# Optimization experiments

Measured on AMD Instinct MI355X. Metric: run time of the kernel, lower is better.

The kernel has to match this reference:

```python
import jax, jax.numpy as jnp
import numpy as np

N = 100000
E = 800000
D_IN = 128
D_OUT = 128


def setup_inputs() -> dict:
    key = jax.random.key(0)
    k1, k2, k3, k4, k5 = jax.random.split(key, 5)
    x = jax.random.normal(k1, (N, D_IN), dtype=jnp.float32)
    edge_index = jax.random.randint(k2, (2, E), 0, N, dtype=jnp.int64)
    # xavier-uniform linear weight [out, in]
    lim_w = float(np.sqrt(6.0 / (D_IN + D_OUT)))
    lin_w = jax.random.uniform(k3, (D_OUT, D_IN), minval=-lim_w, maxval=lim_w, dtype=jnp.float32)
    # torch default bias init: U(-1/sqrt(fan_in), 1/sqrt(fan_in))
    lim_b = float(1.0 / np.sqrt(D_IN))
    lin_b = jax.random.uniform(k4, (D_OUT,), minval=-lim_b, maxval=lim_b, dtype=jnp.float32)
    lim_s = float(np.sqrt(6.0 / (D_OUT + D_OUT)))
    weight = jax.random.uniform(k5, (D_OUT, D_OUT), minval=-lim_s, maxval=lim_s, dtype=jnp.float32)
    return {"x": x, "edge_index": edge_index, "lin_w": lin_w, "lin_b": lin_b, "weight": weight}


def reference(x, edge_index, lin_w, lin_b, weight):
    row, col = edge_index[0], edge_index[1]
    # mean aggregation: scatter-add gathered neighbor features, normalize by degree
    agg = jax.ops.segment_sum(x[col], row, num_segments=x.shape[0])  # [N, d_in]
    deg = jax.ops.segment_sum(jnp.ones_like(row, dtype=x.dtype), row, num_segments=x.shape[0])
    deg = jnp.maximum(deg, 1.0)
    out = agg / deg[:, None]
    out = out @ lin_w.T + lin_b          # linear
    out = out @ weight                    # trailing matmul
    return out
```

## Files before the change

kernel.cpp:

```cpp
#include <hip/hip_runtime.h>

#define N_NODES 100000
#define N_EDGES 800000
#define D 128
#define MAXDEG 40
#define YSTRIDE 132
#define HIST_B 896
#define HIST_T (HIST_B * 256)
#define TILES 3125
#define TB2 1563

typedef unsigned int u32;
typedef unsigned short u16;
typedef __attribute__((ext_vector_type(8))) short bf16x8;
typedef __attribute__((ext_vector_type(4))) float f32x4;

static __device__ __forceinline__ short f2bf(float f) {
    u32 u = __float_as_uint(f);
    u += 0x7FFFu + ((u >> 16) & 1u);
    return (short)(u >> 16);
}
static __device__ __forceinline__ u32 pack2(float lo, float hi) {
    return (u32)(u16)f2bf(lo) | ((u32)(u16)f2bf(hi) << 16);
}
static __device__ __forceinline__ float bf_lo(u32 u) { return __uint_as_float(u << 16); }
static __device__ __forceinline__ float bf_hi(u32 u) { return __uint_as_float(u & 0xFFFF0000u); }

__global__ __launch_bounds__(256) void hist_pre_kernel(
    const int* __restrict__ ei,
    const float* __restrict__ lin_w, const float* __restrict__ lin_b,
    const float* __restrict__ weight,
    u32* __restrict__ deg16, int* __restrict__ csr,
    u16* __restrict__ Mfrag, float* __restrict__ b2)
{
    int t = threadIdx.x;
    int blk = blockIdx.x;
    if (blk < HIST_B) {
        int e0 = blk * 256 + t;
        int e1 = e0 + HIST_T;
        int e2 = e0 + 2 * HIST_T;
        int e3 = e0 + 3 * HIST_T;
        int r0 = ei[e0];
        int r1 = ei[e1];
        int r2 = ei[e2];
        bool has3 = (e3 < N_EDGES);
        int r3 = has3 ? ei[e3] : 0;
        int c0 = ei[N_EDGES + e0];
        int c1 = ei[N_EDGES + e1];
        int c2 = ei[N_EDGES + e2];
        int c3 = has3 ? ei[N_EDGES + e3] : 0;
        u32 p0 = atomicAdd(deg16 + r0 * 16, 1u);
        u32 p1 = atomicAdd(deg16 + r1 * 16, 1u);
        u32 p2 = atomicAdd(deg16 + r2 * 16, 1u);
        u32 p3 = has3 ? atomicAdd(deg16 + r3 * 16, 1u) : (u32)MAXDEG;
        if (p0 < (u32)MAXDEG) csr[r0 * MAXDEG + (int)p0] = c0;
        if (p1 < (u32)MAXDEG) csr[r1 * MAXDEG + (int)p1] = c1;
        if (p2 < (u32)MAXDEG) csr[r2 * MAXDEG + (int)p2] = c2;
        if (p3 < (u32)MAXDEG) csr[r3 * MAXDEG + (int)p3] = c3;
    } else if (blk < 960) {
        int kk = (blk - HIST_B) * 2 + (t >> 7);
        int n = t & 127;
        float acc = 0.f;
        for (int o = 0; o < D; ++o)
            acc += lin_w[o * D + kk] * weight[o * D + n];
        int idx = ((((n >> 4) * 4 + (kk >> 5)) * 64) + ((kk >> 3) & 3) * 16 + (n & 15)) * 8 + (kk & 7);
        Mfrag[idx] = (u16)f2bf(acc);
    } else if (blk == 960 && t < D) {
        float acc = 0.f;
        for (int o = 0; o < D; ++o)
            acc += lin_b[o] * weight[o * D + t];
        b2[t] = acc;
    }
}

static __device__ __forceinline__ void compute_tile(
    const char* __restrict__ bufb, float* __restrict__ shY,
    const bf16x8* __restrict__ mb, u16* __restrict__ y,
    int tile, int t, int rt, int ch, int quad, int mrow, int sw)
{
    int r = rt * 16 + mrow;
    f32x4 acc0 = {0.f, 0.f, 0.f, 0.f};
    f32x4 acc1 = {0.f, 0.f, 0.f, 0.f};
    f32x4 acc2 = {0.f, 0.f, 0.f, 0.f};
    f32x4 acc3 = {0.f, 0.f, 0.f, 0.f};

    #pragma unroll
    for (int ks = 0; ks < 4; ++ks) {
        int base = quad * 32 + ks * 128;
        float4 lo = *(const float4*)(bufb + (r << 9) + (base ^ sw));
        float4 hi = *(const float4*)(bufb + (r << 9) + ((base + 16) ^ sw));
        bf16x8 a;
        a[0] = f2bf(lo.x); a[1] = f2bf(lo.y); a[2] = f2bf(lo.z); a[3] = f2bf(lo.w);
        a[4] = f2bf(hi.x); a[5] = f2bf(hi.y); a[6] = f2bf(hi.z); a[7] = f2bf(hi.w);

        bf16x8 b0 = mb[ks * 64 + 0 * 256];
        bf16x8 b1 = mb[ks * 64 + 1 * 256];
        bf16x8 b2f = mb[ks * 64 + 2 * 256];
        bf16x8 b3 = mb[ks * 64 + 3 * 256];
        acc0 = __builtin_amdgcn_mfma_f32_16x16x32_bf16(a, b0, acc0, 0, 0, 0);
        acc1 = __builtin_amdgcn_mfma_f32_16x16x32_bf16(a, b1, acc1, 0, 0, 0);
        acc2 = __builtin_amdgcn_mfma_f32_16x16x32_bf16(a, b2f, acc2, 0, 0, 0);
        acc3 = __builtin_amdgcn_mfma_f32_16x16x32_bf16(a, b3, acc3, 0, 0, 0);
    }

    {
        float* dst = shY + (size_t)(rt * 16 + quad * 4) * YSTRIDE + ch * 64 + mrow;
        #pragma unroll
        for (int rr = 0; rr < 4; ++rr) {
            dst[rr * YSTRIDE + 0 * 16] = acc0[rr];
            dst[rr * YSTRIDE + 1 * 16] = acc1[rr];
            dst[rr * YSTRIDE + 2 * 16] = acc2[rr];
            dst[rr * YSTRIDE + 3 * 16] = acc3[rr];
        }
    }
    __syncthreads();

    {
        int orow = t >> 3, seg = t & 7;
        const float* src = shY + (size_t)orow * YSTRIDE + seg * 16;
        u32 p[8];
        #pragma unroll
        for (int i = 0; i < 8; ++i)
            p[i] = pack2(src[2 * i], src[2 * i + 1]);
        u32* dst = (u32*)y + ((size_t)(tile * 32 + orow) * 64 + seg * 8);
        *(uint4*)(dst + 0) = make_uint4(p[0], p[1], p[2], p[3]);
        *(uint4*)(dst + 4) = make_uint4(p[4], p[5], p[6], p[7]);
    }
}

__global__ __launch_bounds__(256) void transform_kernel(
    const float* __restrict__ x, const u16* __restrict__ Mfrag, u16* __restrict__ y)
{
    __shared__ float shX[2 * 32 * 128];
    __shared__ float shY[32 * YSTRIDE];
    int t = threadIdx.x;
    int blk = blockIdx.x;
    int wave = t >> 6, lane = t & 63;
    int rt = wave & 1, ch = wave >> 1;
    int quad = lane >> 4, mrow = lane & 15;
    int sw = (mrow & 7) << 4;

    int tile0 = blk * 2;
    int tile1 = blk * 2 + 1;
    bool has1 = (tile1 < TILES);

    {
        char* shXb = (char*)shX;
        #pragma unroll
        for (int i = 0; i < 4; ++i) {
            int s = (i * 256 + t) * 16;
            int rr = s >> 9;
            int cb = s & 511;
            int g = (rr << 9) + (cb ^ ((rr & 7) << 4));
            __builtin_amdgcn_global_load_lds(
                (const u32*)((const char*)x + (size_t)tile0 * 16384 + g),
                (u32*)(shXb + i * 4096 + wave * 1024), 16, 0, 0);
        }
        if (has1) {
            #pragma unroll
            for (int i = 0; i < 4; ++i) {
                int s = (i * 256 + t) * 16;
                int rr = s >> 9;
                int cb = s & 511;
                int g = (rr << 9) + (cb ^ ((rr & 7) << 4));
                __builtin_amdgcn_global_load_lds(
                    (const u32*)((const char*)x + (size_t)tile1 * 16384 + g),
                    (u32*)(shXb + 16384 + i * 4096 + wave * 1024), 16, 0, 0);
            }
        }
    }

    const bf16x8* mb = (const bf16x8*)(Mfrag) + (ch * 4) * 4 * 64 + lane;

    if (has1) asm volatile("s_waitcnt vmcnt(4)" ::: "memory");
    else      asm volatile("s_waitcnt vmcnt(0)" ::: "memory");
    __builtin_amdgcn_s_barrier();
    __builtin_amdgcn_sched_barrier(0);

    compute_tile((const char*)shX, shY, mb, y, tile0, t, rt, ch, quad, mrow, sw);

    if (has1) {
        __syncthreads();
        compute_tile((const char*)shX + 16384, shY, mb, y, tile1, t, rt, ch, quad, mrow, sw);
    }
}

__global__ __launch_bounds__(256) void gather_kernel(
    const u16* __restrict__ y, const int* __restrict__ csr,
    const u32* __restrict__ deg16,
    const float* __restrict__ b2, float* __restrict__ out)
{
    int idx = blockIdx.x * 256 + threadIdx.x;
    int n = idx >> 4;
    int sl = idx & 15;
    if (n >= N_NODES) return;
    u32 dn = deg16[n * 16];
    u32 cnt = (dn > (u32)MAXDEG) ? (u32)MAXDEG : dn;
    const int* cp = csr + (size_t)n * MAXDEG;
    const u32* yw = (const u32*)y;
    float a0 = 0.f, a1 = 0.f, a2 = 0.f, a3 = 0.f;
    float a4 = 0.f, a5 = 0.f, a6 = 0.f, a7 = 0.f;
    u32 e = 0;
    for (; e + 8 <= cnt; e += 8) {
        int4 ca = *(const int4*)(cp + e);
        int4 cb = *(const int4*)(cp + e + 4);
        uint4 u0 = *(const uint4*)(yw + (size_t)ca.x * 64 + sl * 4);
        uint4 u1 = *(const uint4*)(yw + (size_t)ca.y * 64 + sl * 4);
        uint4 u2 = *(const uint4*)(yw + (size_t)ca.z * 64 + sl * 4);
        uint4 u3 = *(const uint4*)(yw + (size_t)ca.w * 64 + sl * 4);
        uint4 u4 = *(const uint4*)(yw + (size_t)cb.x * 64 + sl * 4);
        uint4 u5 = *(const uint4*)(yw + (size_t)cb.y * 64 + sl * 4);
        uint4 u6 = *(const uint4*)(yw + (size_t)cb.z * 64 + sl * 4);
        uint4 u7 = *(const uint4*)(yw + (size_t)cb.w * 64 + sl * 4);
        a0 += ((bf_lo(u0.x) + bf_lo(u1.x)) + (bf_lo(u2.x) + bf_lo(u3.x)))
            + ((bf_lo(u4.x) + bf_lo(u5.x)) + (bf_lo(u6.x) + bf_lo(u7.x)));
        a1 += ((bf_hi(u0.x) + bf_hi(u1.x)) + (bf_hi(u2.x) + bf_hi(u3.x)))
            + ((bf_hi(u4.x) + bf_hi(u5.x)) + (bf_hi(u6.x) + bf_hi(u7.x)));
        a2 += ((bf_lo(u0.y) + bf_lo(u1.y)) + (bf_lo(u2.y) + bf_lo(u3.y)))
            + ((bf_lo(u4.y) + bf_lo(u5.y)) + (bf_lo(u6.y) + bf_lo(u7.y)));
        a3 += ((bf_hi(u0.y) + bf_hi(u1.y)) + (bf_hi(u2.y) + bf_hi(u3.y)))
            + ((bf_hi(u4.y) + bf_hi(u5.y)) + (bf_hi(u6.y) + bf_hi(u7.y)));
        a4 += ((bf_lo(u0.z) + bf_lo(u1.z)) + (bf_lo(u2.z) + bf_lo(u3.z)))
            + ((bf_lo(u4.z) + bf_lo(u5.z)) + (bf_lo(u6.z) + bf_lo(u7.z)));
        a5 += ((bf_hi(u0.z) + bf_hi(u1.z)) + (bf_hi(u2.z) + bf_hi(u3.z)))
            + ((bf_hi(u4.z) + bf_hi(u5.z)) + (bf_hi(u6.z) + bf_hi(u7.z)));
        a6 += ((bf_lo(u0.w) + bf_lo(u1.w)) + (bf_lo(u2.w) + bf_lo(u3.w)))
            + ((bf_lo(u4.w) + bf_lo(u5.w)) + (bf_lo(u6.w) + bf_lo(u7.w)));
        a7 += ((bf_hi(u0.w) + bf_hi(u1.w)) + (bf_hi(u2.w) + bf_hi(u3.w)))
            + ((bf_hi(u4.w) + bf_hi(u5.w)) + (bf_hi(u6.w) + bf_hi(u7.w)));
    }
    for (; e + 4 <= cnt; e += 4) {
        int4 ca = *(const int4*)(cp + e);
        uint4 u0 = *(const uint4*)(yw + (size_t)ca.x * 64 + sl * 4);
        uint4 u1 = *(const uint4*)(yw + (size_t)ca.y * 64 + sl * 4);
        uint4 u2 = *(const uint4*)(yw + (size_t)ca.z * 64 + sl * 4);
        uint4 u3 = *(const uint4*)(yw + (size_t)ca.w * 64 + sl * 4);
        a0 += (bf_lo(u0.x) + bf_lo(u1.x)) + (bf_lo(u2.x) + bf_lo(u3.x));
        a1 += (bf_hi(u0.x) + bf_hi(u1.x)) + (bf_hi(u2.x) + bf_hi(u3.x));
        a2 += (bf_lo(u0.y) + bf_lo(u1.y)) + (bf_lo(u2.y) + bf_lo(u3.y));
        a3 += (bf_hi(u0.y) + bf_hi(u1.y)) + (bf_hi(u2.y) + bf_hi(u3.y));
        a4 += (bf_lo(u0.z) + bf_lo(u1.z)) + (bf_lo(u2.z) + bf_lo(u3.z));
        a5 += (bf_hi(u0.z) + bf_hi(u1.z)) + (bf_hi(u2.z) + bf_hi(u3.z));
        a6 += (bf_lo(u0.w) + bf_lo(u1.w)) + (bf_lo(u2.w) + bf_lo(u3.w));
        a7 += (bf_hi(u0.w) + bf_hi(u1.w)) + (bf_hi(u2.w) + bf_hi(u3.w));
    }
    for (; e < cnt; ++e) {
        uint4 u0 = *(const uint4*)(yw + (size_t)cp[e] * 64 + sl * 4);
        a0 += bf_lo(u0.x); a1 += bf_hi(u0.x);
        a2 += bf_lo(u0.y); a3 += bf_hi(u0.y);
        a4 += bf_lo(u0.z); a5 += bf_hi(u0.z);
        a6 += bf_lo(u0.w); a7 += bf_hi(u0.w);
    }
    float inv = 1.0f / (float)((dn < 1u) ? 1u : dn);
    float4 bA = *(const float4*)(b2 + sl * 8);
    float4 bB = *(const float4*)(b2 + sl * 8 + 4);
    float4 oA, oB;
    oA.x = a0 * inv + bA.x;
    oA.y = a1 * inv + bA.y;
    oA.z = a2 * inv + bA.z;
    oA.w = a3 * inv + bA.w;
    oB.x = a4 * inv + bB.x;
    oB.y = a5 * inv + bB.y;
    oB.z = a6 * inv + bB.z;
    oB.w = a7 * inv + bB.w;
    float* op = out + (size_t)n * D + sl * 8;
    *(float4*)(op + 0) = oA;
    *(float4*)(op + 4) = oB;
}

extern "C" void kernel_launch(void* const* d_in, const int* in_sizes, int n_in,
                              void* d_out, int out_size, void* d_ws, size_t ws_size,
                              hipStream_t stream) {
    const float* x      = (const float*)d_in[0];
    const int*   ei     = (const int*)d_in[1];
    const float* lin_w  = (const float*)d_in[2];
    const float* lin_b  = (const float*)d_in[3];
    const float* weight = (const float*)d_in[4];
    float* out = (float*)d_out;

    char* ws = (char*)d_ws;
    const size_t YB2 = (size_t)N_NODES * D * sizeof(u16);
    const size_t DB  = (size_t)N_NODES * 16 * sizeof(u32);
    u16*   y     = (u16*)ws;
    u32*   deg16 = (u32*)(ws + YB2);
    u16*   Mfrag = (u16*)(ws + YB2 + DB);
    float* b2    = (float*)(ws + YB2 + DB + 32768);
    int*   csr   = (int*)(ws + YB2 + DB + 32768 + 512);

    hipMemsetAsync(deg16, 0, DB, stream);

    hist_pre_kernel<<<961, 256, 0, stream>>>(ei, lin_w, lin_b, weight, deg16, csr, Mfrag, b2);
    transform_kernel<<<TB2, 256, 0, stream>>>(x, Mfrag, y);
    gather_kernel<<<(N_NODES * 16 + 255) / 256, 256, 0, stream>>>(y, csr, deg16, b2, out);
}
```

Before: 202.4 us.

## Fuse edge histogram/CSR build into transform kernel and fold memset into pre kernel

The degree-zeroing memset is folded into the weight-precompute kernel. Edge histogram atomics and CSR scatter are moved into the transform kernel so their latency overlaps the MFMA tile work, and the B fragments are hoisted into registers once per block. The tile mapping changes to blk and blk+1600, and the 2-tile LDS staging now waits on all loads before starting. This removes one launch and one memset, at the cost of more register pressure and the loss of the earlier partial-wait overlap between the two tiles.

```diff
diff --git a/kernel.cpp b/kernel.cpp
--- a/kernel.cpp
+++ b/kernel.cpp
@@ -5,10 +5,10 @@
 #define D 128
 #define MAXDEG 40
 #define YSTRIDE 132
-#define HIST_B 896
-#define HIST_T (HIST_B * 256)
+#define FUSE_B 1600
+#define FULL_B 1525
 #define TILES 3125
-#define TB2 1563
+#define PRE_Z 1563
 
 typedef unsigned int u32;
 typedef unsigned short u16;
@@ -26,46 +26,34 @@
 static __device__ __forceinline__ float bf_lo(u32 u) { return __uint_as_float(u << 16); }
 static __device__ __forceinline__ float bf_hi(u32 u) { return __uint_as_float(u & 0xFFFF0000u); }
 
-__global__ __launch_bounds__(256) void hist_pre_kernel(
-    const int* __restrict__ ei,
+static __device__ __forceinline__ void barrier_keep_vm() {
+    __builtin_amdgcn_sched_barrier(0);
+    asm volatile("s_waitcnt lgkmcnt(0)" ::: "memory");
+    __builtin_amdgcn_s_barrier();
+    __builtin_amdgcn_sched_barrier(0);
+}
+
+__global__ __launch_bounds__(256) void pre_kernel(
     const float* __restrict__ lin_w, const float* __restrict__ lin_b,
     const float* __restrict__ weight,
-    u32* __restrict__ deg16, int* __restrict__ csr,
-    u16* __restrict__ Mfrag, float* __restrict__ b2)
+    u32* __restrict__ deg16, u16* __restrict__ Mfrag, float* __restrict__ b2)
 {
     int t = threadIdx.x;
     int blk = blockIdx.x;
-    if (blk < HIST_B) {
-        int e0 = blk * 256 + t;
-        int e1 = e0 + HIST_T;
-        int e2 = e0 + 2 * HIST_T;
-        int e3 = e0 + 3 * HIST_T;
-        int r0 = ei[e0];
-        int r1 = ei[e1];
-        int r2 = ei[e2];
-        bool has3 = (e3 < N_EDGES);
-        int r3 = has3 ? ei[e3] : 0;
-        int c0 = ei[N_EDGES + e0];
-        int c1 = ei[N_EDGES + e1];
-        int c2 = ei[N_EDGES + e2];
-        int c3 = has3 ? ei[N_EDGES + e3] : 0;
-        u32 p0 = atomicAdd(deg16 + r0 * 16, 1u);
-        u32 p1 = atomicAdd(deg16 + r1 * 16, 1u);
-        u32 p2 = atomicAdd(deg16 + r2 * 16, 1u);
-        u32 p3 = has3 ? atomicAdd(deg16 + r3 * 16, 1u) : (u32)MAXDEG;
-        if (p0 < (u32)MAXDEG) csr[r0 * MAXDEG + (int)p0] = c0;
-        if (p1 < (u32)MAXDEG) csr[r1 * MAXDEG + (int)p1] = c1;
-        if (p2 < (u32)MAXDEG) csr[r2 * MAXDEG + (int)p2] = c2;
-        if (p3 < (u32)MAXDEG) csr[r3 * MAXDEG + (int)p3] = c3;
-    } else if (blk < 960) {
-        int kk = (blk - HIST_B) * 2 + (t >> 7);
+    if (blk < PRE_Z) {
+        int base = blk * 1024 + t * 4;
+        #pragma unroll
+        for (int k = 0; k < 4; ++k)
+            if (base + k < N_NODES * 16) deg16[base + k] = 0u;
+    } else if (blk < PRE_Z + 64) {
+        int kk = (blk - PRE_Z) * 2 + (t >> 7);
         int n = t & 127;
         float acc = 0.f;
         for (int o = 0; o < D; ++o)
             acc += lin_w[o * D + kk] * weight[o * D + n];
         int idx = ((((n >> 4) * 4 + (kk >> 5)) * 64) + ((kk >> 3) & 3) * 16 + (n & 15)) * 8 + (kk & 7);
         Mfrag[idx] = (u16)f2bf(acc);
-    } else if (blk == 960 && t < D) {
+    } else if (blk == PRE_Z + 64 && t < D) {
         float acc = 0.f;
         for (int o = 0; o < D; ++o)
             acc += lin_b[o] * weight[o * D + t];
@@ -73,9 +61,26 @@
     }
 }
 
-static __device__ __forceinline__ void compute_tile(
+static __device__ __forceinline__ void stage_tile(
+    const float* __restrict__ x, int tile, float* __restrict__ shX,
+    int t, int wave)
+{
+    char* shXb = (char*)shX;
+    #pragma unroll
+    for (int i = 0; i < 4; ++i) {
+        int s = (i * 256 + t) * 16;
+        int rr = s >> 9;
+        int cb = s & 511;
+        int g = (rr << 9) + (cb ^ ((rr & 7) << 4));
+        __builtin_amdgcn_global_load_lds(
+            (const u32*)((const char*)x + (size_t)tile * 16384 + g),
+            (u32*)(shXb + i * 4096 + wave * 1024), 16, 0, 0);
+    }
+}
+
+static __device__ __forceinline__ void compute_tile_raw(
     const char* __restrict__ bufb, float* __restrict__ shY,
-    const bf16x8* __restrict__ mb, u16* __restrict__ y,
+    const bf16x8* __restrict__ bf, u16* __restrict__ y,
     int tile, int t, int rt, int ch, int quad, int mrow, int sw)
 {
     int r = rt * 16 + mrow;
@@ -93,14 +98,10 @@
         a[0] = f2bf(lo.x); a[1] = f2bf(lo.y); a[2] = f2bf(lo.z); a[3] = f2bf(lo.w);
         a[4] = f2bf(hi.x); a[5] = f2bf(hi.y); a[6] = f2bf(hi.z); a[7] = f2bf(hi.w);
 
-        bf16x8 b0 = mb[ks * 64 + 0 * 256];
-        bf16x8 b1 = mb[ks * 64 + 1 * 256];
-        bf16x8 b2f = mb[ks * 64 + 2 * 256];
-        bf16x8 b3 = mb[ks * 64 + 3 * 256];
-        acc0 = __builtin_amdgcn_mfma_f32_16x16x32_bf16(a, b0, acc0, 0, 0, 0);
-        acc1 = __builtin_amdgcn_mfma_f32_16x16x32_bf16(a, b1, acc1, 0, 0, 0);
-        acc2 = __builtin_amdgcn_mfma_f32_16x16x32_bf16(a, b2f, acc2, 0, 0, 0);
-        acc3 = __builtin_amdgcn_mfma_f32_16x16x32_bf16(a, b3, acc3, 0, 0, 0);
+        acc0 = __builtin_amdgcn_mfma_f32_16x16x32_bf16(a, bf[ks * 4 + 0], acc0, 0, 0, 0);
+        acc1 = __builtin_amdgcn_mfma_f32_16x16x32_bf16(a, bf[ks * 4 + 1], acc1, 0, 0, 0);
+        acc2 = __builtin_amdgcn_mfma_f32_16x16x32_bf16(a, bf[ks * 4 + 2], acc2, 0, 0, 0);
+        acc3 = __builtin_amdgcn_mfma_f32_16x16x32_bf16(a, bf[ks * 4 + 3], acc3, 0, 0, 0);
     }
 
     {
@@ -113,7 +114,7 @@
             dst[rr * YSTRIDE + 3 * 16] = acc3[rr];
         }
     }
-    __syncthreads();
+    barrier_keep_vm();
 
     {
         int orow = t >> 3, seg = t & 7;
@@ -128,10 +129,13 @@
     }
 }
 
-__global__ __launch_bounds__(256) void transform_kernel(
-    const float* __restrict__ x, const u16* __restrict__ Mfrag, u16* __restrict__ y)
-{
-    __shared__ float shX[2 * 32 * 128];
+__global__ __launch_bounds__(256) void fused_kernel(
+    const int* __restrict__ ei, const float* __restrict__ x,
+    u32* __restrict__ deg16, int* __restrict__ csr,
+    const u16* __restrict__ Mfrag, u16* __restrict__ y)
+{
+    __shared__ float shX0[32 * 128];
+    __shared__ float shX1[32 * 128];
     __shared__ float shY[32 * YSTRIDE];
     int t = threadIdx.x;
     int blk = blockIdx.x;
@@ -139,50 +143,48 @@
     int rt = wave & 1, ch = wave >> 1;
     int quad = lane >> 4, mrow = lane & 15;
     int sw = (mrow & 7) << 4;
-
-    int tile0 = blk * 2;
-    int tile1 = blk * 2 + 1;
-    bool has1 = (tile1 < TILES);
-
-    {
-        char* shXb = (char*)shX;
-        #pragma unroll
-        for (int i = 0; i < 4; ++i) {
-            int s = (i * 256 + t) * 16;
-            int rr = s >> 9;
-            int cb = s & 511;
-            int g = (rr << 9) + (cb ^ ((rr & 7) << 4));
-            __builtin_amdgcn_global_load_lds(
-                (const u32*)((const char*)x + (size_t)tile0 * 16384 + g),
-                (u32*)(shXb + i * 4096 + wave * 1024), 16, 0, 0);
-        }
-        if (has1) {
-            #pragma unroll
-            for (int i = 0; i < 4; ++i) {
-                int s = (i * 256 + t) * 16;
-                int rr = s >> 9;
-                int cb = s & 511;
-                int g = (rr << 9) + (cb ^ ((rr & 7) << 4));
-                __builtin_amdgcn_global_load_lds(
-                    (const u32*)((const char*)x + (size_t)tile1 * 16384 + g),
-                    (u32*)(shXb + 16384 + i * 4096 + wave * 1024), 16, 0, 0);
-            }
-        }
-    }
-
-    const bf16x8* mb = (const bf16x8*)(Mfrag) + (ch * 4) * 4 * 64 + lane;
-
-    if (has1) asm volatile("s_waitcnt vmcnt(4)" ::: "memory");
-    else      asm volatile("s_waitcnt vmcnt(0)" ::: "memory");
+    bool full = (blk < FULL_B);
+    int tile0 = blk, tile1 = blk + FUSE_B;
+
+    int e0 = blk * 256 + t;
+    int r0 = ei[e0];
+    int c0 = ei[N_EDGES + e0];
+    int r1 = 0, c1 = 0;
+    if (full) {
+        int e1 = e0 + FUSE_B * 256;
+        r1 = ei[e1];
+        c1 = ei[N_EDGES + e1];
+    }
+
+    const bf16x8* mb = (const bf16x8*)Mfrag + (ch * 4) * 4 * 64 + lane;
+    bf16x8 bf[16];
+    #pragma unroll
+    for (int ks = 0; ks < 4; ++ks)
+        #pragma unroll
+        for (int j = 0; j < 4; ++j)
+            bf[ks * 4 + j] = mb[ks * 64 + j * 256];
+
+    stage_tile(x, tile0, shX0, t, wave);
+    if (full) stage_tile(x, tile1, shX1, t, wave);
+
+    __builtin_amdgcn_sched_barrier(0);
+    asm volatile("s_waitcnt vmcnt(0)" ::: "memory");
     __builtin_amdgcn_s_barrier();
     __builtin_amdgcn_sched_barrier(0);
 
-    compute_tile((const char*)shX, shY, mb, y, tile0, t, rt, ch, quad, mrow, sw);
-
-    if (has1) {
-        __syncthreads();
-        compute_tile((const char*)shX + 16384, shY, mb, y, tile1, t, rt, ch, quad, mrow, sw);
-    }
+    u32 p0 = atomicAdd(deg16 + r0 * 16, 1u);
+    u32 p1 = full ? atomicAdd(deg16 + r1 * 16, 1u) : (u32)MAXDEG;
+    __builtin_amdgcn_sched_barrier(0);
+
+    compute_tile_raw((const char*)shX0, shY, bf, y, tile0, t, rt, ch, quad, mrow, sw);
+
+    if (full) {
+        barrier_keep_vm();
+        compute_tile_raw((const char*)shX1, shY, bf, y, tile1, t, rt, ch, quad, mrow, sw);
+    }
+
+    if (p0 < (u32)MAXDEG) csr[r0 * MAXDEG + (int)p0] = c0;
+    if (full && p1 < (u32)MAXDEG) csr[r1 * MAXDEG + (int)p1] = c1;
 }
 
 __global__ __launch_bounds__(256) void gather_kernel(
@@ -287,9 +289,7 @@
     float* b2    = (float*)(ws + YB2 + DB + 32768);
     int*   csr   = (int*)(ws + YB2 + DB + 32768 + 512);
 
-    hipMemsetAsync(deg16, 0, DB, stream);
-
-    hist_pre_kernel<<<961, 256, 0, stream>>>(ei, lin_w, lin_b, weight, deg16, csr, Mfrag, b2);
-    transform_kernel<<<TB2, 256, 0, stream>>>(x, Mfrag, y);
+    pre_kernel<<<PRE_Z + 65, 256, 0, stream>>>(lin_w, lin_b, weight, deg16, Mfrag, b2);
+    fused_kernel<<<FUSE_B, 256, 0, stream>>>(ei, x, deg16, csr, Mfrag, y);
     gather_kernel<<<(N_NODES * 16 + 255) / 256, 256, 0, stream>>>(y, csr, deg16, b2, out);
 }
```

New measurement: 192.3 us. -5.0%, faster.
